# Optimization experiments

Hardware: AMD Instinct MI355X
Metric: run time of the kernel (lower is better)

The kernel has to match this reference:

```python
import jax, jax.numpy as jnp
import numpy as np

N, H, W = 8, 64, 64
CIN = 512    # latent_size_prev == conv_insize
COUT = 512   # latent_size == conv_outsize
Z = 512      # latent vector dim


def setup_inputs() -> dict:
    key = jax.random.key(0)
    ks = jax.random.split(key, 6)
    data = jax.random.normal(ks[0], (N, H, W, CIN), dtype=jnp.float32)
    latent = jax.random.normal(ks[1], (N, Z), dtype=jnp.float32)
    dense_w = jax.random.normal(ks[2], (Z, CIN), dtype=jnp.float32)
    dense_b = jnp.ones((CIN,), dtype=jnp.float32)  # ones_initializer per StyleBlock2
    conv_w = jax.random.normal(ks[3], (3, 3, CIN, COUT), dtype=jnp.float32)
    bias = jnp.zeros((1, 1, 1, COUT), dtype=jnp.float32)
    noise_coef = jnp.zeros((1, 1, 1, COUT), dtype=jnp.float32)
    noise = jax.random.normal(ks[4], (N, H, W, COUT), dtype=jnp.float32)
    return {"data": data, "latent": latent, "dense_w": dense_w, "dense_b": dense_b,
            "conv_w": conv_w, "bias": bias, "noise_coef": noise_coef, "noise": noise}


def reference(data, latent, dense_w, dense_b, conv_w, bias, noise_coef, noise):
    # ScaledDense: style vector s = latent @ (W * sqrt(2/Z)) + b
    dense_coef = jnp.sqrt(2.0 / Z).astype(data.dtype)
    s = latent @ (dense_w * dense_coef) + dense_b           # [N, CIN]

    # modulate input by style
    x = data * s[:, None, None, :]                          # [N,H,W,CIN]

    conv_coef = jnp.sqrt(2.0 / (CIN * 9)).astype(data.dtype)
    w = conv_w * conv_coef                                  # [3,3,CIN,COUT]
    y = jax.lax.conv_general_dilated(
        x, w, window_strides=(1, 1), padding='SAME',
        dimension_numbers=('NHWC', 'HWIO', 'NHWC'))         # [N,H,W,COUT]

    # demodulation: sum_{k,k,cin} (w * s)^2 == (s^2) @ sum_{k,k} w^2
    w2 = jnp.sum(w * w, axis=(0, 1))                        # [CIN, COUT]
    d = jax.lax.rsqrt((s * s) @ w2 + 1e-8)                  # [N, COUT]
    y = y * d[:, None, None, :]

    y = y + bias + noise * noise_coef
    return jnp.where(y >= 0, y, 0.2 * y)  # leaky relu, alpha=0.2
```

## Files before the change

### kernel.cpp

```cpp
#include <hip/hip_runtime.h>
#include <stdint.h>

typedef unsigned short ushort_t;
typedef unsigned int uint_t;
typedef __bf16 bf16x8 __attribute__((ext_vector_type(8)));
typedef float f32x4 __attribute__((ext_vector_type(4)));

#define C2F 0.02083333333333333f

__device__ __forceinline__ float bf2f(unsigned short u) {
  union { unsigned int i; float f; } v; v.i = ((unsigned int)u) << 16; return v.f;
}
__device__ __forceinline__ unsigned short f2bf(float f) {
  union { float f; unsigned int i; } v; v.f = f;
  unsigned int r = v.i + 0x7FFFu + ((v.i >> 16) & 1u);
  return (unsigned short)(r >> 16);
}
__device__ __forceinline__ bool bf_mode(const void* dense_b) {
  return *(const uint_t*)dense_b == 0x3F803F80u;
}
__device__ __forceinline__ void async16(const void* g, void* l) {
  __builtin_amdgcn_global_load_lds(
      (const __attribute__((address_space(1))) unsigned int*)g,
      (__attribute__((address_space(3))) unsigned int*)l, 16, 0, 0);
}

__global__ void k_style_p(const void* __restrict__ latent, const void* __restrict__ dw,
                          const void* __restrict__ db, float* __restrict__ sp) {
  const bool bf = bf_mode(db);
  int c = blockIdx.x * 256 + threadIdx.x;
  int n = blockIdx.y, zc = blockIdx.z;
  int z0 = zc * 64;
  float acc = 0.f;
  if (bf) {
    const ushort_t* L = (const ushort_t*)latent;
    const ushort_t* W = (const ushort_t*)dw;
    for (int z = z0; z < z0 + 64; ++z) acc += bf2f(L[n * 512 + z]) * bf2f(W[z * 512 + c]);
  } else {
    const float* L = (const float*)latent;
    const float* W = (const float*)dw;
    for (int z = z0; z < z0 + 64; ++z) acc += L[n * 512 + z] * W[z * 512 + c];
  }
  sp[(zc * 8 + n) * 512 + c] = acc;
}

__global__ void k_style_f(const float* __restrict__ sp, const void* __restrict__ db,
                          float* __restrict__ s) {
  const bool bf = bf_mode(db);
  int c = blockIdx.x * 256 + threadIdx.x;
  int n = blockIdx.y;
  float acc = 0.f;
#pragma unroll
  for (int zc = 0; zc < 8; ++zc) acc += sp[(zc * 8 + n) * 512 + c];
  float bv = bf ? bf2f(((const ushort_t*)db)[c]) : ((const float*)db)[c];
  s[n * 512 + c] = acc * 0.0625f + bv;
}

__global__ void k_w2(const void* __restrict__ cw, const void* __restrict__ db,
                     float* __restrict__ w2) {
  const bool bf = bf_mode(db);
  int i = blockIdx.x * blockDim.x + threadIdx.x;
  float a = 0.f;
  if (bf) {
    const ushort_t* W = (const ushort_t*)cw;
    for (int t = 0; t < 9; ++t) { float v = bf2f(W[t * 262144 + i]); a += v * v; }
  } else {
    const float* W = (const float*)cw;
    for (int t = 0; t < 9; ++t) { float v = W[t * 262144 + i]; a += v * v; }
  }
  w2[i] = a;
}

__global__ void k_demod_p(const float* __restrict__ s, const float* __restrict__ w2,
                          float* __restrict__ qp) {
  int c = blockIdx.x * 256 + threadIdx.x;
  int n = blockIdx.y, kc = blockIdx.z;
  int k0 = kc * 64;
  float q = 0.f;
  for (int k = k0; k < k0 + 64; ++k) {
    float sv = s[n * 512 + k];
    q += sv * sv * w2[k * 512 + c];
  }
  qp[(kc * 8 + n) * 512 + c] = q;
}

__global__ void k_demod_f(const float* __restrict__ qp, float* __restrict__ dfac) {
  int c = blockIdx.x * 256 + threadIdx.x;
  int n = blockIdx.y;
  float q = 0.f;
#pragma unroll
  for (int kc = 0; kc < 8; ++kc) q += qp[(kc * 8 + n) * 512 + c];
  dfac[n * 512 + c] = C2F * rsqrtf(C2F * C2F * q + 1e-8f);
}

__global__ void k_wt(const void* __restrict__ cw, const void* __restrict__ db,
                     ushort_t* __restrict__ wT) {
  __shared__ ushort_t tile[64][66];
  const bool bf = bf_mode(db);
  int tap = blockIdx.z;
  int ci0 = blockIdx.y * 64, co0 = blockIdx.x * 64;
  int col = threadIdx.x & 63, r0 = threadIdx.x >> 6;
  if (bf) {
    const ushort_t* src = (const ushort_t*)cw + tap * 262144;
    for (int r = r0; r < 64; r += 4) tile[r][col] = src[(ci0 + r) * 512 + co0 + col];
  } else {
    const float* src = (const float*)cw + tap * 262144;
    for (int r = r0; r < 64; r += 4) tile[r][col] = f2bf(src[(ci0 + r) * 512 + co0 + col]);
  }
  __syncthreads();
  ushort_t* dst = wT + tap * 262144;
  for (int r = r0; r < 64; r += 4)
    dst[(co0 + r) * 512 + ci0 + col] = tile[col][r];
}

__global__ void k_xpad(const void* __restrict__ data, const void* __restrict__ db,
                       const float* __restrict__ s, ushort_t* __restrict__ xpad) {
  const bool bf = bf_mode(db);
  int idx = blockIdx.x * blockDim.x + threadIdx.x;
  int cpair = idx & 255;
  int p = idx >> 8;
  int wp = p % 66; int q = p / 66; int hp = q % 66; int n = q / 66;
  uint_t outv = 0u;
  if ((unsigned)(hp - 1) < 64u && (unsigned)(wp - 1) < 64u) {
    int c = cpair * 2;
    int src = ((n * 64 + (hp - 1)) * 64 + (wp - 1)) * 512 + c;
    float s0 = s[n * 512 + c], s1 = s[n * 512 + c + 1];
    float x0, x1;
    if (bf) {
      uint_t dp = *(const uint_t*)((const ushort_t*)data + src);
      x0 = bf2f((unsigned short)(dp & 0xFFFFu)) * s0;
      x1 = bf2f((unsigned short)(dp >> 16)) * s1;
    } else {
      const float* df = (const float*)data;
      x0 = df[src] * s0;
      x1 = df[src + 1] * s1;
    }
    outv = (uint_t)f2bf(x0) | ((uint_t)f2bf(x1) << 16);
  }
  *(uint_t*)(xpad + idx * 2) = outv;
}

template <bool BF>
__device__ __forceinline__ void do_epilogue(
    const f32x4 (&acc)[4][4], const float* __restrict__ dfac,
    const void* __restrict__ bias, const void* __restrict__ ncoef,
    const void* __restrict__ noise, void* __restrict__ out,
    int n_img, int posBase, int coutBase, int lane, int wm, int wn) {
  const int rowq = (lane >> 4) * 4;
#pragma unroll
  for (int j = 0; j < 4; ++j) {
    const int cout = coutBase + wn + j * 16 + (lane & 15);
    const float dv = dfac[n_img * 512 + cout];
    const float bv = BF ? bf2f(((const ushort_t*)bias)[cout]) : ((const float*)bias)[cout];
    const float nc = BF ? bf2f(((const ushort_t*)ncoef)[cout]) : ((const float*)ncoef)[cout];
#pragma unroll
    for (int i = 0; i < 4; ++i) {
      const int m = wm + i * 16 + rowq;
#pragma unroll
      for (int r = 0; r < 4; ++r) {
        const size_t o = (size_t)(posBase + m + r) * 512 + cout;
        const float nv = BF ? bf2f(((const ushort_t*)noise)[o]) : ((const float*)noise)[o];
        float y = acc[i][j][r] * dv + bv + nv * nc;
        y = (y >= 0.f) ? y : 0.2f * y;
        if (BF) ((ushort_t*)out)[o] = f2bf(y);
        else    ((float*)out)[o] = y;
      }
    }
  }
}

__global__ __launch_bounds__(256, 2) void k_conv(
    const ushort_t* __restrict__ xpad, const ushort_t* __restrict__ wT,
    const float* __restrict__ dfac, const void* __restrict__ bias,
    const void* __restrict__ ncoef, const void* __restrict__ noise,
    const void* __restrict__ db, void* __restrict__ out) {
  __shared__ ushort_t Asm[128 * 32];
  __shared__ ushort_t Bsm[128 * 32];

  const int t = threadIdx.x;
  const int bid = blockIdx.x;
  const int xcd = bid & 7;
  const int slot = bid >> 3;
  const int coutBase = (slot & 3) * 128;
  const int posBase = ((slot >> 2) + 32 * xcd) * 128;
  const int n_img = posBase >> 12;

  const int prow = t >> 2;
  const int kch = (t & 3) * 8;
  const int pos0 = posBase + prow;
  const int pos1 = pos0 + 64;
  const int h0 = (pos0 >> 6) & 63, w0c = pos0 & 63;
  const int h1 = (pos1 >> 6) & 63, w1c = pos1 & 63;
  const ushort_t* gA0 = xpad + ((n_img * 66 + h0) * 66 + w0c) * 512 + kch;
  const ushort_t* gA1 = xpad + ((n_img * 66 + h1) * 66 + w1c) * 512 + kch;
  const ushort_t* gB0 = wT + (coutBase + prow) * 512 + kch;
  const ushort_t* gB1 = gB0 + 64 * 512;
  ushort_t* lA0 = Asm + t * 8;
  ushort_t* lA1 = lA0 + 64 * 32;
  ushort_t* lB0 = Bsm + t * 8;
  ushort_t* lB1 = lB0 + 64 * 32;

  const int lane = t & 63;
  const int wm = ((t >> 7) & 1) * 64;
  const int wn = ((t >> 6) & 1) * 64;
  const int mrow = lane & 15;
  const int kreg = (lane >> 4) * 8;

  f32x4 acc[4][4] = {};

  for (int tap = 0; tap < 9; ++tap) {
    const int kh = tap / 3, kw = tap - kh * 3;
    const ushort_t* pA0 = gA0 + (kh * 66 + kw) * 512;
    const ushort_t* pA1 = gA1 + (kh * 66 + kw) * 512;
    const ushort_t* pB0 = gB0 + tap * 262144;
    const ushort_t* pB1 = gB1 + tap * 262144;
    for (int k0 = 0; k0 < 512; k0 += 32) {
      async16(pA0 + k0, lA0);
      async16(pA1 + k0, lA1);
      async16(pB0 + k0, lB0);
      async16(pB1 + k0, lB1);
      asm volatile("s_waitcnt vmcnt(0)" ::: "memory");
      __syncthreads();
      bf16x8 av[4], bv[4];
#pragma unroll
      for (int i = 0; i < 4; ++i)
        av[i] = *(const bf16x8*)(Asm + (wm + i * 16 + mrow) * 32 + kreg);
#pragma unroll
      for (int j = 0; j < 4; ++j)
        bv[j] = *(const bf16x8*)(Bsm + (wn + j * 16 + mrow) * 32 + kreg);
#pragma unroll
      for (int i = 0; i < 4; ++i)
#pragma unroll
        for (int j = 0; j < 4; ++j)
          acc[i][j] = __builtin_amdgcn_mfma_f32_16x16x32_bf16(av[i], bv[j], acc[i][j], 0, 0, 0);
      __syncthreads();
    }
  }

  if (bf_mode(db))
    do_epilogue<true>(acc, dfac, bias, ncoef, noise, out, n_img, posBase, coutBase, lane, wm, wn);
  else
    do_epilogue<false>(acc, dfac, bias, ncoef, noise, out, n_img, posBase, coutBase, lane, wm, wn);
}

extern "C" void kernel_launch(void* const* d_in, const int* in_sizes, int n_in,
                              void* d_out, int out_size, void* d_ws, size_t ws_size,
                              hipStream_t stream) {
  (void)in_sizes; (void)n_in; (void)out_size; (void)ws_size;
  const void* data    = d_in[0];
  const void* latent  = d_in[1];
  const void* dense_w = d_in[2];
  const void* dense_b = d_in[3];
  const void* conv_w  = d_in[4];
  const void* bias    = d_in[5];
  const void* ncoef   = d_in[6];
  const void* noise   = d_in[7];

  float* s    = (float*)d_ws;
  float* dfac = s + 4096;
  float* w2   = dfac + 4096;
  float* sp   = w2 + 262144;
  float* qp   = sp + 32768;
  ushort_t* wT   = (ushort_t*)(qp + 32768);
  ushort_t* xpad = wT + 2359296;

  k_style_p<<<dim3(2, 8, 8), 256, 0, stream>>>(latent, dense_w, dense_b, sp);
  k_style_f<<<dim3(2, 8), 256, 0, stream>>>(sp, dense_b, s);
  k_w2<<<1024, 256, 0, stream>>>(conv_w, dense_b, w2);
  k_wt<<<dim3(8, 8, 9), 256, 0, stream>>>(conv_w, dense_b, wT);
  k_demod_p<<<dim3(2, 8, 8), 256, 0, stream>>>(s, w2, qp);
  k_demod_f<<<dim3(2, 8), 256, 0, stream>>>(qp, dfac);
  k_xpad<<<34848, 256, 0, stream>>>(data, dense_b, s, xpad);
  k_conv<<<1024, 256, 0, stream>>>(xpad, wT, dfac, bias, ncoef, noise, dense_b, d_out);
}
```

Baseline: 434.2 us.

## Fuse prep kernels, vectorize xpad, and widen conv K-tile with swizzled LDS

Merges the weight transpose and squared-weight sum into one kernel, and the style and demodulation computations into another, cutting the launch count from eight to four. The padding/modulation kernel now moves eight channels per thread with 16-byte loads and stores. The conv kernel doubles its K step to 64 with XOR-swizzled LDS layout to avoid bank conflicts and halve barrier count, and raises launch bounds occupancy hint. Risks include lower parallelism in the small prep kernels (k_wprep 64 blocks, k_sd 8 blocks) and register pressure from the tighter launch bound.

```diff
diff --git a/kernel.cpp b/kernel.cpp
--- a/kernel.cpp
+++ b/kernel.cpp
@@ -25,119 +25,99 @@
       (__attribute__((address_space(3))) unsigned int*)l, 16, 0, 0);
 }
 
-__global__ void k_style_p(const void* __restrict__ latent, const void* __restrict__ dw,
-                          const void* __restrict__ db, float* __restrict__ sp) {
+__global__ void k_wprep(const void* __restrict__ cw, const void* __restrict__ db,
+                        ushort_t* __restrict__ wT, float* __restrict__ w2) {
+  __shared__ ushort_t tile[64][66];
   const bool bf = bf_mode(db);
-  int c = blockIdx.x * 256 + threadIdx.x;
-  int n = blockIdx.y, zc = blockIdx.z;
-  int z0 = zc * 64;
+  const int co0 = blockIdx.x * 64, ci0 = blockIdx.y * 64;
+  const int col = threadIdx.x & 63, r0 = threadIdx.x >> 6;
+  float w2a[16];
+#pragma unroll
+  for (int i = 0; i < 16; ++i) w2a[i] = 0.f;
+  for (int tap = 0; tap < 9; ++tap) {
+    if (tap) __syncthreads();
+    int i = 0;
+#pragma unroll
+    for (int rr = r0; rr < 64; rr += 4, ++i) {
+      float v;
+      if (bf) {
+        ushort_t u = ((const ushort_t*)cw)[tap * 262144 + (ci0 + rr) * 512 + co0 + col];
+        tile[rr][col] = u; v = bf2f(u);
+      } else {
+        float f = ((const float*)cw)[tap * 262144 + (ci0 + rr) * 512 + co0 + col];
+        tile[rr][col] = f2bf(f); v = f;
+      }
+      w2a[i] += v * v;
+    }
+    __syncthreads();
+#pragma unroll
+    for (int rr = r0; rr < 64; rr += 4)
+      wT[tap * 262144 + (co0 + rr) * 512 + ci0 + col] = tile[col][rr];
+  }
+  int i = 0;
+#pragma unroll
+  for (int rr = r0; rr < 64; rr += 4, ++i)
+    w2[(ci0 + rr) * 512 + co0 + col] = w2a[i];
+}
+
+__global__ void k_sd(const void* __restrict__ latent, const void* __restrict__ dw,
+                     const void* __restrict__ db, const float* __restrict__ w2,
+                     float* __restrict__ s, float* __restrict__ dfac) {
+  __shared__ float lat[512];
+  __shared__ float s2[512];
+  const bool bf = bf_mode(db);
+  const int n = blockIdx.x, c = threadIdx.x;
+  lat[c] = bf ? bf2f(((const ushort_t*)latent)[n * 512 + c])
+              : ((const float*)latent)[n * 512 + c];
+  __syncthreads();
   float acc = 0.f;
   if (bf) {
-    const ushort_t* L = (const ushort_t*)latent;
     const ushort_t* W = (const ushort_t*)dw;
-    for (int z = z0; z < z0 + 64; ++z) acc += bf2f(L[n * 512 + z]) * bf2f(W[z * 512 + c]);
+    for (int z = 0; z < 512; ++z) acc += lat[z] * bf2f(W[z * 512 + c]);
   } else {
-    const float* L = (const float*)latent;
     const float* W = (const float*)dw;
-    for (int z = z0; z < z0 + 64; ++z) acc += L[n * 512 + z] * W[z * 512 + c];
-  }
-  sp[(zc * 8 + n) * 512 + c] = acc;
-}
-
-__global__ void k_style_f(const float* __restrict__ sp, const void* __restrict__ db,
-                          float* __restrict__ s) {
-  const bool bf = bf_mode(db);
-  int c = blockIdx.x * 256 + threadIdx.x;
-  int n = blockIdx.y;
-  float acc = 0.f;
-#pragma unroll
-  for (int zc = 0; zc < 8; ++zc) acc += sp[(zc * 8 + n) * 512 + c];
+    for (int z = 0; z < 512; ++z) acc += lat[z] * W[z * 512 + c];
+  }
   float bv = bf ? bf2f(((const ushort_t*)db)[c]) : ((const float*)db)[c];
-  s[n * 512 + c] = acc * 0.0625f + bv;
-}
-
-__global__ void k_w2(const void* __restrict__ cw, const void* __restrict__ db,
-                     float* __restrict__ w2) {
-  const bool bf = bf_mode(db);
-  int i = blockIdx.x * blockDim.x + threadIdx.x;
-  float a = 0.f;
-  if (bf) {
-    const ushort_t* W = (const ushort_t*)cw;
-    for (int t = 0; t < 9; ++t) { float v = bf2f(W[t * 262144 + i]); a += v * v; }
-  } else {
-    const float* W = (const float*)cw;
-    for (int t = 0; t < 9; ++t) { float v = W[t * 262144 + i]; a += v * v; }
-  }
-  w2[i] = a;
-}
-
-__global__ void k_demod_p(const float* __restrict__ s, const float* __restrict__ w2,
-                          float* __restrict__ qp) {
-  int c = blockIdx.x * 256 + threadIdx.x;
-  int n = blockIdx.y, kc = blockIdx.z;
-  int k0 = kc * 64;
-  float q = 0.f;
-  for (int k = k0; k < k0 + 64; ++k) {
-    float sv = s[n * 512 + k];
-    q += sv * sv * w2[k * 512 + c];
-  }
-  qp[(kc * 8 + n) * 512 + c] = q;
-}
-
-__global__ void k_demod_f(const float* __restrict__ qp, float* __restrict__ dfac) {
-  int c = blockIdx.x * 256 + threadIdx.x;
-  int n = blockIdx.y;
-  float q = 0.f;
-#pragma unroll
-  for (int kc = 0; kc < 8; ++kc) q += qp[(kc * 8 + n) * 512 + c];
-  dfac[n * 512 + c] = C2F * rsqrtf(C2F * C2F * q + 1e-8f);
-}
-
-__global__ void k_wt(const void* __restrict__ cw, const void* __restrict__ db,
-                     ushort_t* __restrict__ wT) {
-  __shared__ ushort_t tile[64][66];
-  const bool bf = bf_mode(db);
-  int tap = blockIdx.z;
-  int ci0 = blockIdx.y * 64, co0 = blockIdx.x * 64;
-  int col = threadIdx.x & 63, r0 = threadIdx.x >> 6;
-  if (bf) {
-    const ushort_t* src = (const ushort_t*)cw + tap * 262144;
-    for (int r = r0; r < 64; r += 4) tile[r][col] = src[(ci0 + r) * 512 + co0 + col];
-  } else {
-    const float* src = (const float*)cw + tap * 262144;
-    for (int r = r0; r < 64; r += 4) tile[r][col] = f2bf(src[(ci0 + r) * 512 + co0 + col]);
-  }
+  float sv = acc * 0.0625f + bv;
+  s[n * 512 + c] = sv;
+  s2[c] = sv * sv;
   __syncthreads();
-  ushort_t* dst = wT + tap * 262144;
-  for (int r = r0; r < 64; r += 4)
-    dst[(co0 + r) * 512 + ci0 + col] = tile[col][r];
+  float qv = 0.f;
+  for (int k = 0; k < 512; ++k) qv += s2[k] * w2[k * 512 + c];
+  dfac[n * 512 + c] = C2F * rsqrtf(C2F * C2F * qv + 1e-8f);
 }
 
 __global__ void k_xpad(const void* __restrict__ data, const void* __restrict__ db,
                        const float* __restrict__ s, ushort_t* __restrict__ xpad) {
   const bool bf = bf_mode(db);
-  int idx = blockIdx.x * blockDim.x + threadIdx.x;
-  int cpair = idx & 255;
-  int p = idx >> 8;
-  int wp = p % 66; int q = p / 66; int hp = q % 66; int n = q / 66;
-  uint_t outv = 0u;
+  const int idx = blockIdx.x * 256 + threadIdx.x;
+  const int cg = idx & 63;
+  const int p = idx >> 6;
+  const int wp = p % 66; const int t2 = p / 66; const int hp = t2 % 66; const int n = t2 / 66;
+  uint4 ov = make_uint4(0u, 0u, 0u, 0u);
   if ((unsigned)(hp - 1) < 64u && (unsigned)(wp - 1) < 64u) {
-    int c = cpair * 2;
-    int src = ((n * 64 + (hp - 1)) * 64 + (wp - 1)) * 512 + c;
-    float s0 = s[n * 512 + c], s1 = s[n * 512 + c + 1];
-    float x0, x1;
+    const int c = cg * 8;
+    const long src = ((long)((n * 64 + (hp - 1)) * 64 + (wp - 1))) * 512 + c;
+    float xv[8];
     if (bf) {
-      uint_t dp = *(const uint_t*)((const ushort_t*)data + src);
-      x0 = bf2f((unsigned short)(dp & 0xFFFFu)) * s0;
-      x1 = bf2f((unsigned short)(dp >> 16)) * s1;
+      uint4 d = *(const uint4*)((const ushort_t*)data + src);
+      const ushort_t* du = (const ushort_t*)&d;
+#pragma unroll
+      for (int i = 0; i < 8; ++i) xv[i] = bf2f(du[i]);
     } else {
-      const float* df = (const float*)data;
-      x0 = df[src] * s0;
-      x1 = df[src + 1] * s1;
-    }
-    outv = (uint_t)f2bf(x0) | ((uint_t)f2bf(x1) << 16);
-  }
-  *(uint_t*)(xpad + idx * 2) = outv;
+      const float* dp = (const float*)data + src;
+      float4 a = *(const float4*)dp, b = *(const float4*)(dp + 4);
+      xv[0] = a.x; xv[1] = a.y; xv[2] = a.z; xv[3] = a.w;
+      xv[4] = b.x; xv[5] = b.y; xv[6] = b.z; xv[7] = b.w;
+    }
+    const float* sp = s + n * 512 + c;
+    ushort_t ou[8];
+#pragma unroll
+    for (int i = 0; i < 8; ++i) ou[i] = f2bf(xv[i] * sp[i]);
+    ov = *(const uint4*)ou;
+  }
+  *(uint4*)(xpad + (size_t)idx * 8) = ov;
 }
 
 template <bool BF>
@@ -169,13 +149,13 @@
   }
 }
 
-__global__ __launch_bounds__(256, 2) void k_conv(
+__global__ __launch_bounds__(256, 4) void k_conv(
     const ushort_t* __restrict__ xpad, const ushort_t* __restrict__ wT,
     const float* __restrict__ dfac, const void* __restrict__ bias,
     const void* __restrict__ ncoef, const void* __restrict__ noise,
     const void* __restrict__ db, void* __restrict__ out) {
-  __shared__ ushort_t Asm[128 * 32];
-  __shared__ ushort_t Bsm[128 * 32];
+  __shared__ ushort_t Asm[128 * 64];
+  __shared__ ushort_t Bsm[128 * 64];
 
   const int t = threadIdx.x;
   const int bid = blockIdx.x;
@@ -185,54 +165,59 @@
   const int posBase = ((slot >> 2) + 32 * xcd) * 128;
   const int n_img = posBase >> 12;
 
-  const int prow = t >> 2;
-  const int kch = (t & 3) * 8;
-  const int pos0 = posBase + prow;
-  const int pos1 = pos0 + 64;
-  const int h0 = (pos0 >> 6) & 63, w0c = pos0 & 63;
-  const int h1 = (pos1 >> 6) & 63, w1c = pos1 & 63;
-  const ushort_t* gA0 = xpad + ((n_img * 66 + h0) * 66 + w0c) * 512 + kch;
-  const ushort_t* gA1 = xpad + ((n_img * 66 + h1) * 66 + w1c) * 512 + kch;
-  const ushort_t* gB0 = wT + (coutBase + prow) * 512 + kch;
-  const ushort_t* gB1 = gB0 + 64 * 512;
-  ushort_t* lA0 = Asm + t * 8;
-  ushort_t* lA1 = lA0 + 64 * 32;
-  ushort_t* lB0 = Bsm + t * 8;
-  ushort_t* lB1 = lB0 + 64 * 32;
+  const int r = t >> 3;
+  const int gc = (t & 7) ^ (r & 7);
+  const int kch = gc * 8;
+
+  const ushort_t* gA[4];
+  const ushort_t* gB[4];
+#pragma unroll
+  for (int s4 = 0; s4 < 4; ++s4) {
+    const int pos = posBase + r + 32 * s4;
+    const int h = (pos >> 6) & 63, w = pos & 63;
+    gA[s4] = xpad + ((n_img * 66 + h) * 66 + w) * 512 + kch;
+    gB[s4] = wT + (coutBase + r + 32 * s4) * 512 + kch;
+  }
+  ushort_t* lA = Asm + t * 8;
+  ushort_t* lB = Bsm + t * 8;
 
   const int lane = t & 63;
   const int wm = ((t >> 7) & 1) * 64;
   const int wn = ((t >> 6) & 1) * 64;
   const int mrow = lane & 15;
-  const int kreg = (lane >> 4) * 8;
+  const int q4 = lane >> 4;
+  const int sw = mrow & 7;
 
   f32x4 acc[4][4] = {};
 
   for (int tap = 0; tap < 9; ++tap) {
     const int kh = tap / 3, kw = tap - kh * 3;
-    const ushort_t* pA0 = gA0 + (kh * 66 + kw) * 512;
-    const ushort_t* pA1 = gA1 + (kh * 66 + kw) * 512;
-    const ushort_t* pB0 = gB0 + tap * 262144;
-    const ushort_t* pB1 = gB1 + tap * 262144;
-    for (int k0 = 0; k0 < 512; k0 += 32) {
-      async16(pA0 + k0, lA0);
-      async16(pA1 + k0, lA1);
-      async16(pB0 + k0, lB0);
-      async16(pB1 + k0, lB1);
+    const int aoff = (kh * 66 + kw) * 512;
+    const int boff = tap * 262144;
+    for (int k0 = 0; k0 < 512; k0 += 64) {
+#pragma unroll
+      for (int s4 = 0; s4 < 4; ++s4) {
+        async16(gA[s4] + aoff + k0, lA + s4 * 2048);
+        async16(gB[s4] + boff + k0, lB + s4 * 2048);
+      }
       asm volatile("s_waitcnt vmcnt(0)" ::: "memory");
       __syncthreads();
-      bf16x8 av[4], bv[4];
-#pragma unroll
-      for (int i = 0; i < 4; ++i)
-        av[i] = *(const bf16x8*)(Asm + (wm + i * 16 + mrow) * 32 + kreg);
-#pragma unroll
-      for (int j = 0; j < 4; ++j)
-        bv[j] = *(const bf16x8*)(Bsm + (wn + j * 16 + mrow) * 32 + kreg);
-#pragma unroll
-      for (int i = 0; i < 4; ++i)
+#pragma unroll
+      for (int kk = 0; kk < 2; ++kk) {
+        const int ca = ((kk * 4 + q4) ^ sw) * 8;
+        bf16x8 av[4], bv[4];
+#pragma unroll
+        for (int i = 0; i < 4; ++i)
+          av[i] = *(const bf16x8*)(Asm + (wm + i * 16 + mrow) * 64 + ca);
 #pragma unroll
         for (int j = 0; j < 4; ++j)
-          acc[i][j] = __builtin_amdgcn_mfma_f32_16x16x32_bf16(av[i], bv[j], acc[i][j], 0, 0, 0);
+          bv[j] = *(const bf16x8*)(Bsm + (wn + j * 16 + mrow) * 64 + ca);
+#pragma unroll
+        for (int i = 0; i < 4; ++i)
+#pragma unroll
+          for (int j = 0; j < 4; ++j)
+            acc[i][j] = __builtin_amdgcn_mfma_f32_16x16x32_bf16(av[i], bv[j], acc[i][j], 0, 0, 0);
+      }
       __syncthreads();
     }
   }
@@ -259,17 +244,11 @@
   float* s    = (float*)d_ws;
   float* dfac = s + 4096;
   float* w2   = dfac + 4096;
-  float* sp   = w2 + 262144;
-  float* qp   = sp + 32768;
-  ushort_t* wT   = (ushort_t*)(qp + 32768);
+  ushort_t* wT   = (ushort_t*)(w2 + 262144);
   ushort_t* xpad = wT + 2359296;
 
-  k_style_p<<<dim3(2, 8, 8), 256, 0, stream>>>(latent, dense_w, dense_b, sp);
-  k_style_f<<<dim3(2, 8), 256, 0, stream>>>(sp, dense_b, s);
-  k_w2<<<1024, 256, 0, stream>>>(conv_w, dense_b, w2);
-  k_wt<<<dim3(8, 8, 9), 256, 0, stream>>>(conv_w, dense_b, wT);
-  k_demod_p<<<dim3(2, 8, 8), 256, 0, stream>>>(s, w2, qp);
-  k_demod_f<<<dim3(2, 8), 256, 0, stream>>>(qp, dfac);
-  k_xpad<<<34848, 256, 0, stream>>>(data, dense_b, s, xpad);
+  k_wprep<<<dim3(8, 8), 256, 0, stream>>>(conv_w, dense_b, wT, w2);
+  k_sd<<<8, 512, 0, stream>>>(latent, dense_w, dense_b, w2, s, dfac);
+  k_xpad<<<8712, 256, 0, stream>>>(data, dense_b, s, xpad);
   k_conv<<<1024, 256, 0, stream>>>(xpad, wT, dfac, bias, ncoef, noise, dense_b, d_out);
 }
```

Result: slower. 499.8 us (+15.1%).
